# Kernel optimization log

Measured on AMD Instinct MI355X. Metric: run time of the kernel, lower is better.

## Reference

```python
import jax, jax.numpy as jnp
import numpy as np

ORDER, POINTS, N = 3, 16, 2048
D1, D2, POOL1, POOL2, LABELS = 64, 32, 32, 8, 10


def setup_inputs() -> dict:
    key = jax.random.key(0)
    ks = jax.random.split(key, 8)
    adj = jax.random.uniform(ks[0], (ORDER, N, N), dtype=jnp.float32)  # normalized adjacency powers
    # original inits weight_matrix uniform(-1000, 1000)
    wm = jax.random.uniform(ks[1], (ORDER, POINTS), dtype=jnp.float32, minval=-1000.0, maxval=1000.0)
    w1 = jax.random.normal(ks[2], (ORDER * POINTS, D1), dtype=jnp.float32) * 0.1
    b1 = jnp.zeros((D1,), jnp.float32)
    w2 = jax.random.normal(ks[3], (D1, D2), dtype=jnp.float32) * 0.1
    b2 = jnp.zeros((D2,), jnp.float32)
    p1 = jax.random.normal(ks[4], (D2, POOL1), dtype=jnp.float32) * 0.1
    pb1 = jnp.zeros((POOL1,), jnp.float32)
    p2 = jax.random.normal(ks[5], (POOL1, POOL2), dtype=jnp.float32) * 0.1
    pb2 = jnp.zeros((POOL2,), jnp.float32)
    cw = jax.random.normal(ks[6], (POOL2 * D2, LABELS), dtype=jnp.float32) * 0.1
    cb = jnp.zeros((LABELS,), jnp.float32)
    return dict(adj=adj, wm=wm, w1=w1, b1=b1, w2=w2, b2=b2,
                p1=p1, pb1=pb1, p2=p2, pb2=pb2, cw=cw, cb=cb)


def reference(adj, wm, w1, b1, w2, b2, p1, pb1, p2, pb2, cw, cb):
    order, n, _ = adj.shape
    pts = wm.shape[1]
    # LearningToEvaluateLayer: per-order outer product theta ⊗ A, cos, mean over last node dim
    # scores: [order, pts, n, n]; feats: [order, pts, n]
    feats = jnp.mean(jnp.cos(wm[:, :, None, None] * adj[:, None, :, :]), axis=3)
    # torch.t(features) per order then cat along dim=1 -> [n, order*pts]
    ms = jnp.transpose(feats, (2, 0, 1)).reshape(n, order * pts)
    h1 = jax.nn.relu(ms @ w1 + b1)          # [n, D1]
    h2 = jax.nn.relu(h1 @ w2 + b2)          # [n, D2]
    # SagePoolingLayer: attention over nodes (softmax along dim=0)
    abstract = jnp.tanh(h2 @ p1 + pb1)      # [n, POOL1]
    att = jax.nn.softmax(abstract @ p2 + pb2, axis=0)  # [n, POOL2]
    g = (att.T @ h2).reshape(1, -1)         # [1, POOL2*D2]
    logits = g @ cw + cb                    # [1, LABELS]
    return jax.nn.log_softmax(logits, axis=1)
```

## Files before the change

kernel.cpp:

```cpp
#include <hip/hip_runtime.h>
#include <hip/hip_bf16.h>
#include <math.h>

#define ORDER  3
#define POINTS 16
#define NNODES 2048
#define D1 64
#define D2 32
#define POOL1 32
#define POOL2 8
#define LABELS 10
#define PBLK   32

__global__ __launch_bounds__(64) void k_feats(const float* __restrict__ adj,
                                              const float* __restrict__ wm,
                                              float* __restrict__ ms) {
    const int i    = blockIdx.x;
    const int o    = blockIdx.y;
    const int lane = threadIdx.x;

    const float INV2PI = 0.15915494309189535f;
    float wr[POINTS];
#pragma unroll
    for (int p = 0; p < POINTS; ++p)
        wr[p] = wm[o * POINTS + p] * INV2PI;

    const float4* row4 =
        reinterpret_cast<const float4*>(adj + ((size_t)o * NNODES + (size_t)i) * NNODES);

    float acc[POINTS];
#pragma unroll
    for (int p = 0; p < POINTS; ++p) acc[p] = 0.0f;

#pragma unroll
    for (int c = 0; c < NNODES / (4 * 64); ++c) {
        float4 a4 = row4[c * 64 + lane];
        float av[4] = {a4.x, a4.y, a4.z, a4.w};
#pragma unroll
        for (int e = 0; e < 4; ++e) {
            float a = av[e];
#pragma unroll
            for (int p = 0; p < POINTS; ++p) {
                float r = __builtin_amdgcn_fractf(a * wr[p]);
                acc[p] += __builtin_amdgcn_cosf(r);
            }
        }
    }

#pragma unroll
    for (int p = 0; p < POINTS; ++p) {
        float v = acc[p];
#pragma unroll
        for (int off = 32; off >= 1; off >>= 1)
            v += __shfl_xor(v, off, 64);
        acc[p] = v;
    }

    if (lane == 0) {
        float* out = ms + (size_t)i * (ORDER * POINTS) + o * POINTS;
        const float rn = 1.0f / (float)NNODES;
#pragma unroll
        for (int p = 0; p < POINTS; ++p)
            out[p] = acc[p] * rn;
    }
}

__global__ __launch_bounds__(256) void k_mlp(const float* __restrict__ ms,
                                             const float* __restrict__ w1,
                                             const float* __restrict__ b1,
                                             const float* __restrict__ w2,
                                             const float* __restrict__ b2,
                                             const float* __restrict__ p1,
                                             const float* __restrict__ pb1,
                                             const float* __restrict__ p2,
                                             const float* __restrict__ pb2,
                                             float* __restrict__ h2out,
                                             float* __restrict__ sout) {
    const int t  = threadIdx.x;
    const int r0 = blockIdx.x * 32;

    __shared__ float lms[32 * 48];
    __shared__ float lw1[48 * D1];
    __shared__ float lh1[32 * D1];
    __shared__ float lw2[D1 * D2];
    __shared__ float lh2[32 * D2];
    __shared__ float lp1[D2 * POOL1];
    __shared__ float lav[32 * POOL1];
    __shared__ float lp2[POOL1 * POOL2];
    __shared__ float ls[32 * POOL2];
    __shared__ float lb1[D1], lb2[D2], lpb1[POOL1], lpb2[POOL2];

    for (int idx = t; idx < 32 * 48; idx += 256) lms[idx] = ms[(size_t)r0 * 48 + idx];
    for (int idx = t; idx < 48 * D1; idx += 256) lw1[idx] = w1[idx];
    for (int idx = t; idx < D1 * D2; idx += 256) lw2[idx] = w2[idx];
    for (int idx = t; idx < D2 * POOL1; idx += 256) lp1[idx] = p1[idx];
    if (t < POOL1 * POOL2) lp2[t] = p2[t];
    if (t < D1) lb1[t] = b1[t];
    if (t < D2) lb2[t] = b2[t];
    if (t < POOL1) lpb1[t] = pb1[t];
    if (t < POOL2) lpb2[t] = pb2[t];
    __syncthreads();

    {
        const int dim = t & 63;
        const int rg  = t >> 6;
        float acc[8];
#pragma unroll
        for (int j = 0; j < 8; ++j) acc[j] = 0.0f;
#pragma unroll
        for (int k4 = 0; k4 < 12; ++k4) {
            const float wa = lw1[(k4 * 4 + 0) * D1 + dim];
            const float wb = lw1[(k4 * 4 + 1) * D1 + dim];
            const float wc = lw1[(k4 * 4 + 2) * D1 + dim];
            const float wd = lw1[(k4 * 4 + 3) * D1 + dim];
#pragma unroll
            for (int j = 0; j < 8; ++j) {
                const float4 m4 = *reinterpret_cast<const float4*>(&lms[(rg * 8 + j) * 48 + k4 * 4]);
                acc[j] = fmaf(m4.x, wa, fmaf(m4.y, wb, fmaf(m4.z, wc, fmaf(m4.w, wd, acc[j]))));
            }
        }
        const float bb = lb1[dim];
#pragma unroll
        for (int j = 0; j < 8; ++j)
            lh1[(rg * 8 + j) * D1 + dim] = fmaxf(acc[j] + bb, 0.0f);
    }
    __syncthreads();

    {
        const int dim = t & 31;
        const int rg  = t >> 5;
        float acc[4] = {0.0f, 0.0f, 0.0f, 0.0f};
#pragma unroll
        for (int k4 = 0; k4 < 16; ++k4) {
            const float wa = lw2[(k4 * 4 + 0) * D2 + dim];
            const float wb = lw2[(k4 * 4 + 1) * D2 + dim];
            const float wc = lw2[(k4 * 4 + 2) * D2 + dim];
            const float wd = lw2[(k4 * 4 + 3) * D2 + dim];
#pragma unroll
            for (int j = 0; j < 4; ++j) {
                const float4 h4 = *reinterpret_cast<const float4*>(&lh1[(rg * 4 + j) * D1 + k4 * 4]);
                acc[j] = fmaf(h4.x, wa, fmaf(h4.y, wb, fmaf(h4.z, wc, fmaf(h4.w, wd, acc[j]))));
            }
        }
        const float bb = lb2[dim];
#pragma unroll
        for (int j = 0; j < 4; ++j)
            lh2[(rg * 4 + j) * D2 + dim] = fmaxf(acc[j] + bb, 0.0f);
    }
    __syncthreads();

    reinterpret_cast<float4*>(h2out)[(size_t)blockIdx.x * 256 + t] =
        reinterpret_cast<const float4*>(lh2)[t];

    {
        const int dim = t & 31;
        const int rg  = t >> 5;
        float acc[4] = {0.0f, 0.0f, 0.0f, 0.0f};
#pragma unroll
        for (int k4 = 0; k4 < 8; ++k4) {
            const float wa = lp1[(k4 * 4 + 0) * POOL1 + dim];
            const float wb = lp1[(k4 * 4 + 1) * POOL1 + dim];
            const float wc = lp1[(k4 * 4 + 2) * POOL1 + dim];
            const float wd = lp1[(k4 * 4 + 3) * POOL1 + dim];
#pragma unroll
            for (int j = 0; j < 4; ++j) {
                const float4 h4 = *reinterpret_cast<const float4*>(&lh2[(rg * 4 + j) * D2 + k4 * 4]);
                acc[j] = fmaf(h4.x, wa, fmaf(h4.y, wb, fmaf(h4.z, wc, fmaf(h4.w, wd, acc[j]))));
            }
        }
        const float bb = lpb1[dim];
#pragma unroll
        for (int j = 0; j < 4; ++j)
            lav[(rg * 4 + j) * POOL1 + dim] = tanhf(acc[j] + bb);
    }
    __syncthreads();

    {
        const int row = t >> 3;
        const int c   = t & 7;
        float acc = lpb2[c];
#pragma unroll
        for (int k = 0; k < POOL1; ++k)
            acc = fmaf(lav[row * POOL1 + k], lp2[k * POOL2 + c], acc);
        ls[row * POOL2 + c] = acc;
    }
    __syncthreads();

    sout[(size_t)r0 * POOL2 + t] = ls[t];
}

__global__ __launch_bounds__(256) void k_pool(const float* __restrict__ sIn,
                                              const float* __restrict__ h2,
                                              float* __restrict__ part,
                                              float* __restrict__ rinvOut) {
    const int b = blockIdx.x;
    const int t = threadIdx.x;

    __shared__ float red[256];
    __shared__ float colmax[POOL2];
    __shared__ float colsum[POOL2];
    __shared__ float att_l[64 * POOL2];

    const int c  = t & 7;
    const int rg = t >> 3;

    float pm = -1e30f;
    for (int j = 0; j < 64; ++j)
        pm = fmaxf(pm, sIn[(size_t)(rg * 64 + j) * POOL2 + c]);
    red[c * 32 + rg] = pm;
    __syncthreads();
    if (t < POOL2) {
        float m = red[t * 32];
#pragma unroll
        for (int k = 1; k < 32; ++k) m = fmaxf(m, red[t * 32 + k]);
        colmax[t] = m;
    }
    __syncthreads();

    const float mx = colmax[c];
    float ps = 0.0f;
    for (int j = 0; j < 64; ++j)
        ps += expf(sIn[(size_t)(rg * 64 + j) * POOL2 + c] - mx);
    red[c * 32 + rg] = ps;
    __syncthreads();
    if (t < POOL2) {
        float s = 0.0f;
#pragma unroll
        for (int k = 0; k < 32; ++k) s += red[t * 32 + k];
        colsum[t] = s;
        if (b == 0) rinvOut[t] = 1.0f / s;
    }
    __syncthreads();

    for (int idx = t; idx < 64 * POOL2; idx += 256) {
        const int j  = idx >> 3;
        const int cc = idx & 7;
        att_l[idx] = expf(sIn[(size_t)(b * 64 + j) * POOL2 + cc] - colmax[cc]);
    }
    __syncthreads();

    {
        const int c2 = t >> 5;
        const int d  = t & 31;
        float acc = 0.0f;
        for (int j = 0; j < 64; ++j)
            acc = fmaf(att_l[j * POOL2 + c2], h2[(size_t)(b * 64 + j) * D2 + d], acc);
        part[(size_t)b * 256 + t] = acc;
    }
}

__global__ __launch_bounds__(640) void k_logits(const float* __restrict__ part,
                                                const float* __restrict__ rinv8,
                                                const float* __restrict__ cw,
                                                const float* __restrict__ cb,
                                                float* __restrict__ out) {
    const int l    = threadIdx.x >> 6;
    const int lane = threadIdx.x & 63;
    __shared__ float gs[256];
    __shared__ float lg[LABELS];

    if (threadIdx.x < 256) {
        float s = 0.0f;
#pragma unroll
        for (int b = 0; b < PBLK; ++b) s += part[(size_t)b * 256 + threadIdx.x];
        gs[threadIdx.x] = s * rinv8[threadIdx.x >> 5];
    }
    __syncthreads();

    float p = 0.0f;
    for (int k = lane; k < POOL2 * D2; k += 64)
        p = fmaf(gs[k], cw[(size_t)k * LABELS + l], p);
#pragma unroll
    for (int off = 32; off >= 1; off >>= 1)
        p += __shfl_xor(p, off, 64);
    if (lane == 0) lg[l] = p + cb[l];
    __syncthreads();
    if (threadIdx.x == 0) {
        float m = lg[0];
#pragma unroll
        for (int i = 1; i < LABELS; ++i) m = fmaxf(m, lg[i]);
        float se = 0.0f;
#pragma unroll
        for (int i = 0; i < LABELS; ++i) se += expf(lg[i] - m);
        const float lse = m + logf(se);
#pragma unroll
        for (int i = 0; i < LABELS; ++i) out[i] = lg[i] - lse;
    }
}

extern "C" void kernel_launch(void* const* d_in, const int* in_sizes, int n_in,
                              void* d_out, int out_size, void* d_ws, size_t ws_size,
                              hipStream_t stream) {
    const float* adj = (const float*)d_in[0];
    const float* wm  = (const float*)d_in[1];
    const float* w1  = (const float*)d_in[2];
    const float* b1  = (const float*)d_in[3];
    const float* w2  = (const float*)d_in[4];
    const float* b2  = (const float*)d_in[5];
    const float* p1  = (const float*)d_in[6];
    const float* pb1 = (const float*)d_in[7];
    const float* p2  = (const float*)d_in[8];
    const float* pb2 = (const float*)d_in[9];
    const float* cw  = (const float*)d_in[10];
    const float* cb  = (const float*)d_in[11];
    float* out = (float*)d_out;

    float* ws   = (float*)d_ws;
    float* ms   = ws;
    float* h2   = ms + (size_t)NNODES * ORDER * POINTS;
    float* sS   = h2 + (size_t)NNODES * D2;
    float* part = sS + (size_t)NNODES * POOL2;
    float* rinv = part + (size_t)PBLK * 256;

    hipLaunchKernelGGL(k_feats, dim3(NNODES, ORDER), dim3(64), 0, stream, adj, wm, ms);
    hipLaunchKernelGGL(k_mlp, dim3(NNODES / 32), dim3(256), 0, stream,
                       ms, w1, b1, w2, b2, p1, pb1, p2, pb2, h2, sS);
    hipLaunchKernelGGL(k_pool, dim3(PBLK), dim3(256), 0, stream, sS, h2, part, rinv);
    hipLaunchKernelGGL(k_logits, dim3(1), dim3(640), 0, stream, part, rinv, cw, cb, out);
}
```

Baseline: 152.0 us.

## Fuse feature, MLP and pooling stages into fewer kernels with last-block reduction

Merges the cosine feature kernel and the per-node MLP into one kernel, where each block handles one node across all three orders (192 threads) and runs the small MLP chain in shared memory. The logits kernel is folded into the pooling kernel through an atomic counter, so the last block to finish does the final reduction. The feature loop now prefetches the next adjacency chunk in software. This removes two launches and the intermediate feature round trip, in exchange for a memset, MLP weights reloaded from global memory in every block, and mostly idle threads during the MLP phases.

```diff
diff --git a/kernel.cpp b/kernel.cpp
--- a/kernel.cpp
+++ b/kernel.cpp
@@ -12,12 +12,27 @@
 #define LABELS 10
 #define PBLK   32
 
-__global__ __launch_bounds__(64) void k_feats(const float* __restrict__ adj,
+__global__ __launch_bounds__(192) void k_main(const float* __restrict__ adj,
                                               const float* __restrict__ wm,
-                                              float* __restrict__ ms) {
+                                              const float* __restrict__ w1,
+                                              const float* __restrict__ b1,
+                                              const float* __restrict__ w2,
+                                              const float* __restrict__ b2,
+                                              const float* __restrict__ p1,
+                                              const float* __restrict__ pb1,
+                                              const float* __restrict__ p2,
+                                              const float* __restrict__ pb2,
+                                              float* __restrict__ h2out,
+                                              float* __restrict__ sout) {
     const int i    = blockIdx.x;
-    const int o    = blockIdx.y;
-    const int lane = threadIdx.x;
+    const int t    = threadIdx.x;
+    const int o    = t >> 6;
+    const int lane = t & 63;
+
+    __shared__ float lf[ORDER * POINTS];
+    __shared__ float lh1[D1];
+    __shared__ float lh2[D2];
+    __shared__ float lav[POOL1];
 
     const float INV2PI = 0.15915494309189535f;
     float wr[POINTS];
@@ -32,19 +47,20 @@
 #pragma unroll
     for (int p = 0; p < POINTS; ++p) acc[p] = 0.0f;
 
-#pragma unroll
+    float4 cur = row4[lane];
     for (int c = 0; c < NNODES / (4 * 64); ++c) {
-        float4 a4 = row4[c * 64 + lane];
-        float av[4] = {a4.x, a4.y, a4.z, a4.w};
+        const float4 nxt = (c < 7) ? row4[(c + 1) * 64 + lane] : cur;
+        float av4[4] = {cur.x, cur.y, cur.z, cur.w};
 #pragma unroll
         for (int e = 0; e < 4; ++e) {
-            float a = av[e];
+            const float a = av4[e];
 #pragma unroll
             for (int p = 0; p < POINTS; ++p) {
                 float r = __builtin_amdgcn_fractf(a * wr[p]);
                 acc[p] += __builtin_amdgcn_cosf(r);
             }
         }
+        cur = nxt;
     }
 
 #pragma unroll
@@ -53,146 +69,55 @@
 #pragma unroll
         for (int off = 32; off >= 1; off >>= 1)
             v += __shfl_xor(v, off, 64);
-        acc[p] = v;
-    }
-
-    if (lane == 0) {
-        float* out = ms + (size_t)i * (ORDER * POINTS) + o * POINTS;
-        const float rn = 1.0f / (float)NNODES;
-#pragma unroll
-        for (int p = 0; p < POINTS; ++p)
-            out[p] = acc[p] * rn;
-    }
-}
-
-__global__ __launch_bounds__(256) void k_mlp(const float* __restrict__ ms,
-                                             const float* __restrict__ w1,
-                                             const float* __restrict__ b1,
-                                             const float* __restrict__ w2,
-                                             const float* __restrict__ b2,
-                                             const float* __restrict__ p1,
-                                             const float* __restrict__ pb1,
-                                             const float* __restrict__ p2,
-                                             const float* __restrict__ pb2,
-                                             float* __restrict__ h2out,
-                                             float* __restrict__ sout) {
-    const int t  = threadIdx.x;
-    const int r0 = blockIdx.x * 32;
-
-    __shared__ float lms[32 * 48];
-    __shared__ float lw1[48 * D1];
-    __shared__ float lh1[32 * D1];
-    __shared__ float lw2[D1 * D2];
-    __shared__ float lh2[32 * D2];
-    __shared__ float lp1[D2 * POOL1];
-    __shared__ float lav[32 * POOL1];
-    __shared__ float lp2[POOL1 * POOL2];
-    __shared__ float ls[32 * POOL2];
-    __shared__ float lb1[D1], lb2[D2], lpb1[POOL1], lpb2[POOL2];
-
-    for (int idx = t; idx < 32 * 48; idx += 256) lms[idx] = ms[(size_t)r0 * 48 + idx];
-    for (int idx = t; idx < 48 * D1; idx += 256) lw1[idx] = w1[idx];
-    for (int idx = t; idx < D1 * D2; idx += 256) lw2[idx] = w2[idx];
-    for (int idx = t; idx < D2 * POOL1; idx += 256) lp1[idx] = p1[idx];
-    if (t < POOL1 * POOL2) lp2[t] = p2[t];
-    if (t < D1) lb1[t] = b1[t];
-    if (t < D2) lb2[t] = b2[t];
-    if (t < POOL1) lpb1[t] = pb1[t];
-    if (t < POOL2) lpb2[t] = pb2[t];
-    __syncthreads();
-
-    {
-        const int dim = t & 63;
-        const int rg  = t >> 6;
-        float acc[8];
-#pragma unroll
-        for (int j = 0; j < 8; ++j) acc[j] = 0.0f;
-#pragma unroll
-        for (int k4 = 0; k4 < 12; ++k4) {
-            const float wa = lw1[(k4 * 4 + 0) * D1 + dim];
-            const float wb = lw1[(k4 * 4 + 1) * D1 + dim];
-            const float wc = lw1[(k4 * 4 + 2) * D1 + dim];
-            const float wd = lw1[(k4 * 4 + 3) * D1 + dim];
-#pragma unroll
-            for (int j = 0; j < 8; ++j) {
-                const float4 m4 = *reinterpret_cast<const float4*>(&lms[(rg * 8 + j) * 48 + k4 * 4]);
-                acc[j] = fmaf(m4.x, wa, fmaf(m4.y, wb, fmaf(m4.z, wc, fmaf(m4.w, wd, acc[j]))));
-            }
-        }
-        const float bb = lb1[dim];
-#pragma unroll
-        for (int j = 0; j < 8; ++j)
-            lh1[(rg * 8 + j) * D1 + dim] = fmaxf(acc[j] + bb, 0.0f);
-    }
-    __syncthreads();
-
-    {
-        const int dim = t & 31;
-        const int rg  = t >> 5;
-        float acc[4] = {0.0f, 0.0f, 0.0f, 0.0f};
-#pragma unroll
-        for (int k4 = 0; k4 < 16; ++k4) {
-            const float wa = lw2[(k4 * 4 + 0) * D2 + dim];
-            const float wb = lw2[(k4 * 4 + 1) * D2 + dim];
-            const float wc = lw2[(k4 * 4 + 2) * D2 + dim];
-            const float wd = lw2[(k4 * 4 + 3) * D2 + dim];
-#pragma unroll
-            for (int j = 0; j < 4; ++j) {
-                const float4 h4 = *reinterpret_cast<const float4*>(&lh1[(rg * 4 + j) * D1 + k4 * 4]);
-                acc[j] = fmaf(h4.x, wa, fmaf(h4.y, wb, fmaf(h4.z, wc, fmaf(h4.w, wd, acc[j]))));
-            }
-        }
-        const float bb = lb2[dim];
-#pragma unroll
-        for (int j = 0; j < 4; ++j)
-            lh2[(rg * 4 + j) * D2 + dim] = fmaxf(acc[j] + bb, 0.0f);
-    }
-    __syncthreads();
-
-    reinterpret_cast<float4*>(h2out)[(size_t)blockIdx.x * 256 + t] =
-        reinterpret_cast<const float4*>(lh2)[t];
-
-    {
-        const int dim = t & 31;
-        const int rg  = t >> 5;
-        float acc[4] = {0.0f, 0.0f, 0.0f, 0.0f};
-#pragma unroll
-        for (int k4 = 0; k4 < 8; ++k4) {
-            const float wa = lp1[(k4 * 4 + 0) * POOL1 + dim];
-            const float wb = lp1[(k4 * 4 + 1) * POOL1 + dim];
-            const float wc = lp1[(k4 * 4 + 2) * POOL1 + dim];
-            const float wd = lp1[(k4 * 4 + 3) * POOL1 + dim];
-#pragma unroll
-            for (int j = 0; j < 4; ++j) {
-                const float4 h4 = *reinterpret_cast<const float4*>(&lh2[(rg * 4 + j) * D2 + k4 * 4]);
-                acc[j] = fmaf(h4.x, wa, fmaf(h4.y, wb, fmaf(h4.z, wc, fmaf(h4.w, wd, acc[j]))));
-            }
-        }
-        const float bb = lpb1[dim];
-#pragma unroll
-        for (int j = 0; j < 4; ++j)
-            lav[(rg * 4 + j) * POOL1 + dim] = tanhf(acc[j] + bb);
-    }
-    __syncthreads();
-
-    {
-        const int row = t >> 3;
-        const int c   = t & 7;
-        float acc = lpb2[c];
+        if (lane == 0) lf[o * POINTS + p] = v * (1.0f / (float)NNODES);
+    }
+    __syncthreads();
+
+    if (t < D1) {
+        float a = b1[t];
+#pragma unroll
+        for (int k = 0; k < ORDER * POINTS; ++k)
+            a = fmaf(lf[k], w1[(size_t)k * D1 + t], a);
+        lh1[t] = fmaxf(a, 0.0f);
+    }
+    __syncthreads();
+
+    if (t < D2) {
+        float a = b2[t];
+#pragma unroll
+        for (int k = 0; k < D1; ++k)
+            a = fmaf(lh1[k], w2[(size_t)k * D2 + t], a);
+        const float h = fmaxf(a, 0.0f);
+        lh2[t] = h;
+        h2out[(size_t)i * D2 + t] = h;
+    }
+    __syncthreads();
+
+    if (t < POOL1) {
+        float a = pb1[t];
+#pragma unroll
+        for (int k = 0; k < D2; ++k)
+            a = fmaf(lh2[k], p1[(size_t)k * POOL1 + t], a);
+        lav[t] = tanhf(a);
+    }
+    __syncthreads();
+
+    if (t < POOL2) {
+        float a = pb2[t];
 #pragma unroll
         for (int k = 0; k < POOL1; ++k)
-            acc = fmaf(lav[row * POOL1 + k], lp2[k * POOL2 + c], acc);
-        ls[row * POOL2 + c] = acc;
-    }
-    __syncthreads();
-
-    sout[(size_t)r0 * POOL2 + t] = ls[t];
+            a = fmaf(lav[k], p2[(size_t)k * POOL2 + t], a);
+        sout[(size_t)i * POOL2 + t] = a;
+    }
 }
 
 __global__ __launch_bounds__(256) void k_pool(const float* __restrict__ sIn,
                                               const float* __restrict__ h2,
+                                              const float* __restrict__ cw,
+                                              const float* __restrict__ cb,
                                               float* __restrict__ part,
-                                              float* __restrict__ rinvOut) {
+                                              int* __restrict__ counter,
+                                              float* __restrict__ out) {
     const int b = blockIdx.x;
     const int t = threadIdx.x;
 
@@ -200,6 +125,7 @@
     __shared__ float colmax[POOL2];
     __shared__ float colsum[POOL2];
     __shared__ float att_l[64 * POOL2];
+    __shared__ int   sIsLast;
 
     const int c  = t & 7;
     const int rg = t >> 3;
@@ -228,7 +154,6 @@
 #pragma unroll
         for (int k = 0; k < 32; ++k) s += red[t * 32 + k];
         colsum[t] = s;
-        if (b == 0) rinvOut[t] = 1.0f / s;
     }
     __syncthreads();
 
@@ -247,44 +172,39 @@
             acc = fmaf(att_l[j * POOL2 + c2], h2[(size_t)(b * 64 + j) * D2 + d], acc);
         part[(size_t)b * 256 + t] = acc;
     }
-}
-
-__global__ __launch_bounds__(640) void k_logits(const float* __restrict__ part,
-                                                const float* __restrict__ rinv8,
-                                                const float* __restrict__ cw,
-                                                const float* __restrict__ cb,
-                                                float* __restrict__ out) {
-    const int l    = threadIdx.x >> 6;
-    const int lane = threadIdx.x & 63;
+
+    __threadfence();
+    if (t == 0) sIsLast = (atomicAdd(counter, 1) == PBLK - 1);
+    __syncthreads();
+    if (!sIsLast) return;
+    __threadfence();
+
     __shared__ float gs[256];
     __shared__ float lg[LABELS];
-
-    if (threadIdx.x < 256) {
+    {
         float s = 0.0f;
 #pragma unroll
-        for (int b = 0; b < PBLK; ++b) s += part[(size_t)b * 256 + threadIdx.x];
-        gs[threadIdx.x] = s * rinv8[threadIdx.x >> 5];
-    }
-    __syncthreads();
-
-    float p = 0.0f;
-    for (int k = lane; k < POOL2 * D2; k += 64)
-        p = fmaf(gs[k], cw[(size_t)k * LABELS + l], p);
-#pragma unroll
-    for (int off = 32; off >= 1; off >>= 1)
-        p += __shfl_xor(p, off, 64);
-    if (lane == 0) lg[l] = p + cb[l];
-    __syncthreads();
-    if (threadIdx.x == 0) {
+        for (int bb = 0; bb < PBLK; ++bb) s += part[(size_t)bb * 256 + t];
+        gs[t] = s / colsum[t >> 5];
+    }
+    __syncthreads();
+    if (t < LABELS) {
+        float a = cb[t];
+        for (int k = 0; k < POOL2 * D2; ++k)
+            a = fmaf(gs[k], cw[(size_t)k * LABELS + t], a);
+        lg[t] = a;
+    }
+    __syncthreads();
+    if (t == 0) {
         float m = lg[0];
 #pragma unroll
-        for (int i = 1; i < LABELS; ++i) m = fmaxf(m, lg[i]);
+        for (int l = 1; l < LABELS; ++l) m = fmaxf(m, lg[l]);
         float se = 0.0f;
 #pragma unroll
-        for (int i = 0; i < LABELS; ++i) se += expf(lg[i] - m);
+        for (int l = 0; l < LABELS; ++l) se += expf(lg[l] - m);
         const float lse = m + logf(se);
 #pragma unroll
-        for (int i = 0; i < LABELS; ++i) out[i] = lg[i] - lse;
+        for (int l = 0; l < LABELS; ++l) out[l] = lg[l] - lse;
     }
 }
 
@@ -306,15 +226,14 @@
     float* out = (float*)d_out;
 
     float* ws   = (float*)d_ws;
-    float* ms   = ws;
-    float* h2   = ms + (size_t)NNODES * ORDER * POINTS;
+    float* h2   = ws;
     float* sS   = h2 + (size_t)NNODES * D2;
     float* part = sS + (size_t)NNODES * POOL2;
-    float* rinv = part + (size_t)PBLK * 256;
-
-    hipLaunchKernelGGL(k_feats, dim3(NNODES, ORDER), dim3(64), 0, stream, adj, wm, ms);
-    hipLaunchKernelGGL(k_mlp, dim3(NNODES / 32), dim3(256), 0, stream,
-                       ms, w1, b1, w2, b2, p1, pb1, p2, pb2, h2, sS);
-    hipLaunchKernelGGL(k_pool, dim3(PBLK), dim3(256), 0, stream, sS, h2, part, rinv);
-    hipLaunchKernelGGL(k_logits, dim3(1), dim3(640), 0, stream, part, rinv, cw, cb, out);
+    int*  cnt   = (int*)(part + (size_t)PBLK * 256);
+
+    hipMemsetAsync(cnt, 0, sizeof(int), stream);
+    hipLaunchKernelGGL(k_main, dim3(NNODES), dim3(192), 0, stream,
+                       adj, wm, w1, b1, w2, b2, p1, pb1, p2, pb2, h2, sS);
+    hipLaunchKernelGGL(k_pool, dim3(PBLK), dim3(256), 0, stream,
+                       sS, h2, cw, cb, part, cnt, out);
 }
```

Measured after the change: 155.5 us. +2.3%, slower.
